# Kernel tuning notes

Hardware: AMD Instinct MI355X
Metric: run time of the kernel (lower is better)

The kernel has to match this reference:

```python
import jax, jax.numpy as jnp
import numpy as np

H = 2048

def setup_inputs() -> dict:
    key = jax.random.key(0)
    ks = jax.random.split(key, 7)
    s = 1.0 / np.sqrt(H)
    return {
        "input": jax.random.normal(ks[0], (2, 4096, H), dtype=jnp.float32),
        "Wq": jax.random.uniform(ks[1], (H, H), jnp.float32, -s, s),
        "bq": jax.random.uniform(ks[2], (H,), jnp.float32, -s, s),
        "Wk": jax.random.uniform(ks[3], (H, H), jnp.float32, -s, s),
        "bk": jax.random.uniform(ks[4], (H,), jnp.float32, -s, s),
        "Wv": jax.random.uniform(ks[5], (H, H), jnp.float32, -s, s),
        "bv": jax.random.uniform(ks[6], (H,), jnp.float32, -s, s),
    }

def reference(input, Wq, bq, Wk, bk, Wv, bv):
    # Linear projections: y = x @ W^T + b (torch nn.Linear convention)
    q = jnp.einsum('bsh,oh->bso', input, Wq) + bq
    k = jnp.einsum('bsh,oh->bso', input, Wk) + bk
    v = jnp.einsum('bsh,oh->bso', input, Wv) + bv
    # NOTE: original module has NO 1/sqrt(d) scaling and NO mask
    scores = jnp.einsum('bqh,bkh->bqk', q, k)          # [B,S,S]
    attn = jax.nn.softmax(scores, axis=-1)
    out = jnp.einsum('bqk,bkh->bqh', attn, v)           # [B,S,H]
    return out
```

## Files before the change

kernel.cpp:

```cpp
#include <hip/hip_runtime.h>
#include <hip/hip_bf16.h>
#include <cstdint>
#include <cstddef>


typedef _Float16 half8 __attribute__((ext_vector_type(8)));
typedef _Float16 half4 __attribute__((ext_vector_type(4)));
typedef float    f32x4 __attribute__((ext_vector_type(4)));

__device__ __forceinline__ void gld_lds16(const void* g, void* l) {
  __builtin_amdgcn_global_load_lds(
      (const __attribute__((address_space(1))) unsigned int*)g,
      (__attribute__((address_space(3))) unsigned int*)l, 16, 0, 0);
}

#define FENCE()  asm volatile("" ::: "memory")
#define LGKM(n)  asm volatile("s_waitcnt lgkmcnt(" #n ")" ::: "memory")
#define VMC(n)   asm volatile("s_waitcnt vmcnt(" #n ")" ::: "memory")
#define SBAR()   do { __builtin_amdgcn_s_barrier(); FENCE(); } while (0)
#define SCHED0() __builtin_amdgcn_sched_barrier(0)
#define PRIO1()  __builtin_amdgcn_s_setprio(1)
#define PRIO0()  __builtin_amdgcn_s_setprio(0)

#define LOAD_A(dst, RB, MH) do {                                            \
  const char* _p = ldsA + ((RB)*2 + wr) * 16384 + fr * 128;                 \
  _Pragma("unroll") for (int mi = 0; mi < 4; ++mi) {                        \
    dst[mi][0] = *(const half8*)(_p + ((MH)*4 + mi) * 2048 + cS0);          \
    dst[mi][1] = *(const half8*)(_p + ((MH)*4 + mi) * 2048 + cS1);          \
  }                                                                         \
} while (0)

#define LOAD_B(dst, RB, NH) do {                                            \
  const char* _p = ldsB + ((RB)*2 + (wc >> 1)) * 16384 +                    \
                   ((wc & 1) * 64 + fr) * 128;                              \
  _Pragma("unroll") for (int ni = 0; ni < 2; ++ni) {                        \
    dst[ni][0] = *(const half8*)(_p + ((NH)*2 + ni) * 2048 + cS0);          \
    dst[ni][1] = *(const half8*)(_p + ((NH)*2 + ni) * 2048 + cS1);          \
  }                                                                         \
} while (0)

#define MFMA_Q(AF, BF, MH, NH)                                              \
  _Pragma("unroll") for (int mi = 0; mi < 4; ++mi)                          \
  _Pragma("unroll") for (int ni = 0; ni < 2; ++ni) {                        \
    f32x4& _c = acc[(MH)*4 + mi][(NH)*2 + ni];                              \
    _c = __builtin_amdgcn_mfma_f32_16x16x32_f16(AF[mi][0], BF[ni][0], _c, 0, 0, 0); \
    _c = __builtin_amdgcn_mfma_f32_16x16x32_f16(AF[mi][1], BF[ni][1], _c, 0, 0, 0); \
  }

#define STAGE_A(bsel, h, kof)                                               \
  {                                                                         \
    const _Float16* _s = Abase + (size_t)((h) * 128) * lda + (kof);         \
    char* _d = ldsA + ((bsel)*2 + (h)) * 16384 + wvd;                       \
    gld_lds16(_s, _d);                                                      \
    gld_lds16(_s + lda8, _d + 1024);                                        \
  }
#define STAGE_B(bsel, h, kof)                                               \
  {                                                                         \
    const _Float16* _s = Bbase + (size_t)((h) * 128) * ldb + (kof);         \
    char* _d = ldsB + ((bsel)*2 + (h)) * 16384 + wvd;                       \
    gld_lds16(_s, _d);                                                      \
    gld_lds16(_s + ldb8, _d + 1024);                                        \
  }

template <int MODE>
__global__ __launch_bounds__(512) void gemm256(
    const _Float16* __restrict__ A, int lda,
    const _Float16* __restrict__ B, int ldb,
    const float* __restrict__ bias, const float* __restrict__ bias2,
    const float* __restrict__ bias3,
    void* __restrict__ out, void* __restrict__ out2, void* __restrict__ out3,
    int ldo, int K, size_t sA, size_t sB, size_t sO)
{
  __shared__ __attribute__((aligned(128))) char lds[131072];
  char* ldsA = (char*)lds;
  char* ldsB = (char*)lds + 65536;

  const int tid  = threadIdx.x;
  const int wv   = tid >> 6;
  const int lane = tid & 63;
  const int wr = wv >> 2;
  const int wc = wv & 3;
  const int bm = blockIdx.x * 256;
  const int bn = blockIdx.y * 256;
  A += (size_t)blockIdx.z * sA;
  B += (size_t)blockIdx.z * sB;

  const int fr = lane & 15;
  const int kq = lane >> 4;
  const int sx = (fr & 7) << 4;
  const int cS0 = (kq * 16) ^ sx;
  const int cS1 = (64 + kq * 16) ^ sx;
  const int lr  = lane >> 3;
  const int sc8 = ((lane & 7) ^ (lr & 7)) << 3;

  const _Float16* Abase = A + (size_t)(bm + wv * 16 + lr) * lda + sc8;
  const _Float16* Bbase = B + (size_t)(bn + wv * 16 + lr) * ldb + sc8;
  const size_t lda8 = (size_t)lda * 8, ldb8 = (size_t)ldb * 8;
  const int wvd = wv * 2048;

  f32x4 acc[8][4];
  const f32x4 zf = {0.f, 0.f, 0.f, 0.f};
#pragma unroll
  for (int mi = 0; mi < 8; ++mi)
#pragma unroll
    for (int ni = 0; ni < 4; ++ni) acc[mi][ni] = zf;

  half8 af[4][2], bf0[2][2], bf1[2][2];

  const int NT = K >> 6;
  const int NI = NT >> 1;

  STAGE_A(0, 0, 0); STAGE_A(0, 1, 0); STAGE_B(0, 0, 0); STAGE_B(0, 1, 0);
  STAGE_B(1, 0, 64); STAGE_B(1, 1, 64);
  VMC(4);
  SBAR();

  for (int it = 0; it < NI; ++it) {
    const bool more = (it < NI - 1);
    const size_t t1k = (size_t)(2 * it + 1) * 64;
    const size_t t2k = t1k + 64;
    const size_t t3k = t1k + 128;

    LOAD_A(af, 0, 0); LOAD_B(bf0, 0, 0);
    STAGE_A(1, 0, t1k);
    LGKM(8);
    SBAR(); LGKM(0); SCHED0();
    PRIO1(); MFMA_Q(af, bf0, 0, 0); PRIO0();
    SBAR();
    LOAD_B(bf1, 0, 1);
    STAGE_A(1, 1, t1k);
    SBAR(); LGKM(0); SCHED0();
    PRIO1(); MFMA_Q(af, bf1, 0, 1); PRIO0();
    SBAR();
    LOAD_A(af, 0, 1);
    if (more) STAGE_B(0, 0, t2k);
    SBAR(); LGKM(0); SCHED0();
    PRIO1(); MFMA_Q(af, bf1, 1, 1); PRIO0();
    SBAR();
    if (more) STAGE_B(0, 1, t2k);
    SBAR(); SCHED0();
    PRIO1(); MFMA_Q(af, bf0, 1, 0); PRIO0();
    if (more) { VMC(4); } else { VMC(0); }
    SBAR();

    LOAD_A(af, 1, 0); LOAD_B(bf0, 1, 0);
    if (more) STAGE_A(0, 0, t2k);
    LGKM(8);
    SBAR(); LGKM(0); SCHED0();
    PRIO1(); MFMA_Q(af, bf0, 0, 0); PRIO0();
    SBAR();
    LOAD_B(bf1, 1, 1);
    if (more) STAGE_A(0, 1, t2k);
    SBAR(); LGKM(0); SCHED0();
    PRIO1(); MFMA_Q(af, bf1, 0, 1); PRIO0();
    SBAR();
    LOAD_A(af, 1, 1);
    if (more) STAGE_B(1, 0, t3k);
    SBAR(); LGKM(0); SCHED0();
    PRIO1(); MFMA_Q(af, bf1, 1, 1); PRIO0();
    SBAR();
    if (more) STAGE_B(1, 1, t3k);
    SBAR(); SCHED0();
    PRIO1(); MFMA_Q(af, bf0, 1, 0); PRIO0();
    if (more) { VMC(4); } else { VMC(0); }
    SBAR();
  }

  if constexpr (MODE == 1) {
    const int seg = blockIdx.y >> 3;
    const int cb  = (blockIdx.y & 7) * 256;
    _Float16* O; const float* bp;
    if (seg == 0)      { O = (_Float16*)out;  bp = bias;  }
    else if (seg == 1) { O = (_Float16*)out2; bp = bias2; }
    else               { O = (_Float16*)out3; bp = bias3; }
#pragma unroll
    for (int mi = 0; mi < 8; ++mi) {
#pragma unroll
      for (int ni = 0; ni < 4; ++ni) {
        const int colL = cb + wc * 64 + ni * 16 + fr;
        const int row0 = bm + wr * 128 + mi * 16 + kq * 4;
        const f32x4 a = acc[mi][ni];
        const float bb = bp[colL];
        if (seg < 2) {
#pragma unroll
          for (int j = 0; j < 4; ++j)
            O[(size_t)(row0 + j) * 2048 + colL] = (_Float16)(a[j] + bb);
        } else {
          half4 h;
#pragma unroll
          for (int j = 0; j < 4; ++j) h[j] = (_Float16)(a[j] + bb);
          *(half4*)(O + (size_t)colL * 8192 + row0) = h;
        }
      }
    }
  } else {
#pragma unroll
    for (int mi = 0; mi < 8; ++mi) {
#pragma unroll
      for (int ni = 0; ni < 4; ++ni) {
        const int col  = bn + wc * 64 + ni * 16 + fr;
        const int row0 = bm + wr * 128 + mi * 16 + kq * 4;
        const f32x4 a = acc[mi][ni];
        if constexpr (MODE == 0) {
          float* O = (float*)out + (size_t)blockIdx.z * sO;
#pragma unroll
          for (int j = 0; j < 4; ++j) O[(size_t)(row0 + j) * ldo + col] = a[j];
        } else {
          _Float16* O = (_Float16*)out + (size_t)blockIdx.z * sO;
#pragma unroll
          for (int j = 0; j < 4; ++j)
            O[(size_t)(row0 + j) * ldo + col] = (_Float16)a[j];
        }
      }
    }
  }
}

__device__ __forceinline__ float wave_max_f(float v) {
#pragma unroll
  for (int o = 32; o; o >>= 1) v = fmaxf(v, __shfl_xor(v, o));
  return v;
}
__device__ __forceinline__ float wave_sum_f(float v) {
#pragma unroll
  for (int o = 32; o; o >>= 1) v += __shfl_xor(v, o);
  return v;
}

__global__ __launch_bounds__(256) void softmax_rows(
    const _Float16* __restrict__ S, _Float16* __restrict__ P)
{
  __shared__ float rmax[4], rsum[4];
  const int tid = threadIdx.x;
  const _Float16* s = S + (size_t)blockIdx.x * 4096;
  _Float16*       p = P + (size_t)blockIdx.x * 4096;

  const half8 v0 = ((const half8*)s)[tid];
  const half8 v1 = ((const half8*)s)[tid + 256];
  float f[16];
#pragma unroll
  for (int j = 0; j < 8; ++j) { f[j] = (float)v0[j]; f[8 + j] = (float)v1[j]; }

  float m = f[0];
#pragma unroll
  for (int j = 1; j < 16; ++j) m = fmaxf(m, f[j]);
  m = wave_max_f(m);
  if ((tid & 63) == 0) rmax[tid >> 6] = m;
  __syncthreads();
  m = fmaxf(fmaxf(rmax[0], rmax[1]), fmaxf(rmax[2], rmax[3]));

  float sum = 0.f;
#pragma unroll
  for (int j = 0; j < 16; ++j) { f[j] = __expf(f[j] - m); sum += f[j]; }
  sum = wave_sum_f(sum);
  if ((tid & 63) == 0) rsum[tid >> 6] = sum;
  __syncthreads();
  sum = rsum[0] + rsum[1] + rsum[2] + rsum[3];
  const float inv = 1.0f / sum;

  half8 o0, o1;
#pragma unroll
  for (int j = 0; j < 8; ++j) {
    o0[j] = (_Float16)(f[j] * inv);
    o1[j] = (_Float16)(f[8 + j] * inv);
  }
  ((half8*)p)[tid] = o0;
  ((half8*)p)[tid + 256] = o1;
}

__global__ __launch_bounds__(256) void cvt_all(
    const float* __restrict__ X,  const float* __restrict__ Wq,
    const float* __restrict__ Wk, const float* __restrict__ Wv,
    _Float16* __restrict__ dst, int nX4, int nW4)
{
  const int total = nX4 + 3 * nW4;
  const int stride = gridDim.x * 256;
  for (int idx = blockIdx.x * 256 + threadIdx.x; idx < total; idx += stride) {
    const float* src; int off;
    if (idx < nX4)                { src = X;  off = idx; }
    else if (idx < nX4 + nW4)     { src = Wq; off = idx - nX4; }
    else if (idx < nX4 + 2 * nW4) { src = Wk; off = idx - nX4 - nW4; }
    else                          { src = Wv; off = idx - nX4 - 2 * nW4; }
    const f32x4 x = ((const f32x4*)src)[off];
    half4 h;
#pragma unroll
    for (int j = 0; j < 4; ++j) h[j] = (_Float16)x[j];
    ((half4*)dst)[idx] = h;
  }
}

extern "C" void kernel_launch(void* const* d_in, const int* in_sizes, int n_in,
                              void* d_out, int out_size, void* d_ws, size_t ws_size,
                              hipStream_t stream)
{
  const float* X  = (const float*)d_in[0];
  const float* Wq = (const float*)d_in[1];
  const float* bq = (const float*)d_in[2];
  const float* Wk = (const float*)d_in[3];
  const float* bk = (const float*)d_in[4];
  const float* Wv = (const float*)d_in[5];
  const float* bv = (const float*)d_in[6];
  float* out = (float*)d_out;

  const size_t NX = (size_t)2 * 4096 * 2048;
  const size_t NW = (size_t)2048 * 2048;
  const size_t NS = (size_t)2 * 4096 * 4096;

  char* w = (char*)d_ws;
  _Float16* Ssc = (_Float16*)w;
  _Float16* Xh  = (_Float16*)w;
  _Float16* Wc  = (_Float16*)(w + NX * 2);
  _Float16* Q   = (_Float16*)(w + NS * 4);
  _Float16* Kp  = (_Float16*)(w + NS * 4 + NX * 2);
  _Float16* P   = (_Float16*)(w + NS * 4);
  _Float16* Vt  = (_Float16*)(w + NS * 4 + 2 * NX * 2);

  cvt_all<<<2048, 256, 0, stream>>>(X, Wq, Wk, Wv, Xh,
                                    (int)(NX / 4), (int)(NW / 4));

  const dim3 blk(512);
  gemm256<1><<<dim3(32, 24, 1), blk, 0, stream>>>(
      Xh, 2048, Wc, 2048, bq, bk, bv, Q, Kp, Vt, 2048, 2048, 0, 0, 0);
  gemm256<3><<<dim3(16, 16, 2), blk, 0, stream>>>(
      Q, 2048, Kp, 2048, nullptr, nullptr, nullptr, Ssc, nullptr, nullptr,
      4096, 2048, (size_t)4096 * 2048, (size_t)4096 * 2048,
      (size_t)4096 * 4096);
  softmax_rows<<<8192, 256, 0, stream>>>(Ssc, P);
  gemm256<0><<<dim3(16, 8, 2), blk, 0, stream>>>(
      P, 4096, Vt, 8192, nullptr, nullptr, nullptr, out, nullptr, nullptr,
      2048, 4096, (size_t)4096 * 4096, (size_t)4096, (size_t)4096 * 2048);
}
```

Baseline: 477.5 us.

## Switch GEMM inner product from 16x16x32 to 32x32x16 MFMA tiles

Replaces the 16x16x32 f16 MFMA fragments with 32x32x16 MFMA instructions, reorganising LDS fragment loads, accumulator layout (f32x16) and the epilogue index mapping to match. Larger MFMA tiles halve the number of LDS fragment reads per FLOP and reduce instruction issue overhead. The pipeline schedule and barriers are kept the same, with added sched barriers in the prologue. Risks include higher register pressure and different LDS bank-conflict behaviour with the new swizzle offsets.

```diff
diff --git a/kernel.cpp b/kernel.cpp
--- a/kernel.cpp
+++ b/kernel.cpp
@@ -6,7 +6,8 @@
 
 typedef _Float16 half8 __attribute__((ext_vector_type(8)));
 typedef _Float16 half4 __attribute__((ext_vector_type(4)));
-typedef float    f32x4 __attribute__((ext_vector_type(4)));
+typedef float    f32x4  __attribute__((ext_vector_type(4)));
+typedef float    f32x16 __attribute__((ext_vector_type(16)));
 
 __device__ __forceinline__ void gld_lds16(const void* g, void* l) {
   __builtin_amdgcn_global_load_lds(
@@ -22,30 +23,25 @@
 #define PRIO1()  __builtin_amdgcn_s_setprio(1)
 #define PRIO0()  __builtin_amdgcn_s_setprio(0)
 
-#define LOAD_A(dst, RB, MH) do {                                            \
-  const char* _p = ldsA + ((RB)*2 + wr) * 16384 + fr * 128;                 \
-  _Pragma("unroll") for (int mi = 0; mi < 4; ++mi) {                        \
-    dst[mi][0] = *(const half8*)(_p + ((MH)*4 + mi) * 2048 + cS0);          \
-    dst[mi][1] = *(const half8*)(_p + ((MH)*4 + mi) * 2048 + cS1);          \
-  }                                                                         \
+#define LOAD_A32(dst, RB, MP) do {                                          \
+  const char* _p = ldsA + ((RB)*2 + wr) * 16384 + ((MP)*64 + la31) * 128;   \
+  _Pragma("unroll") for (int mi = 0; mi < 2; ++mi)                          \
+    _Pragma("unroll") for (int s = 0; s < 4; ++s)                           \
+      dst[mi][s] = *(const half8*)(_p + mi * 4096 + cK[s]);                 \
 } while (0)
 
-#define LOAD_B(dst, RB, NH) do {                                            \
+#define LOAD_B32(dst, RB, NF) do {                                          \
   const char* _p = ldsB + ((RB)*2 + (wc >> 1)) * 16384 +                    \
-                   ((wc & 1) * 64 + fr) * 128;                              \
-  _Pragma("unroll") for (int ni = 0; ni < 2; ++ni) {                        \
-    dst[ni][0] = *(const half8*)(_p + ((NH)*2 + ni) * 2048 + cS0);          \
-    dst[ni][1] = *(const half8*)(_p + ((NH)*2 + ni) * 2048 + cS1);          \
-  }                                                                         \
+                   ((wc & 1) * 64 + (NF)*32 + la31) * 128;                  \
+  _Pragma("unroll") for (int s = 0; s < 4; ++s)                             \
+    dst[s] = *(const half8*)(_p + cK[s]);                                   \
 } while (0)
 
-#define MFMA_Q(AF, BF, MH, NH)                                              \
-  _Pragma("unroll") for (int mi = 0; mi < 4; ++mi)                          \
-  _Pragma("unroll") for (int ni = 0; ni < 2; ++ni) {                        \
-    f32x4& _c = acc[(MH)*4 + mi][(NH)*2 + ni];                              \
-    _c = __builtin_amdgcn_mfma_f32_16x16x32_f16(AF[mi][0], BF[ni][0], _c, 0, 0, 0); \
-    _c = __builtin_amdgcn_mfma_f32_16x16x32_f16(AF[mi][1], BF[ni][1], _c, 0, 0, 0); \
-  }
+#define MFMAC(MP, AF, BF, NF)                                               \
+  _Pragma("unroll") for (int s = 0; s < 4; ++s)                             \
+  _Pragma("unroll") for (int mi = 0; mi < 2; ++mi)                          \
+    acc32[(MP)*2 + mi][NF] = __builtin_amdgcn_mfma_f32_32x32x16_f16(        \
+        AF[mi][s], BF[s], acc32[(MP)*2 + mi][NF], 0, 0, 0);
 
 #define STAGE_A(bsel, h, kof)                                               \
   {                                                                         \
@@ -85,11 +81,12 @@
   A += (size_t)blockIdx.z * sA;
   B += (size_t)blockIdx.z * sB;
 
-  const int fr = lane & 15;
-  const int kq = lane >> 4;
-  const int sx = (fr & 7) << 4;
-  const int cS0 = (kq * 16) ^ sx;
-  const int cS1 = (64 + kq * 16) ^ sx;
+  const int la31 = lane & 31;
+  const int hi   = lane >> 5;
+  int cK[4];
+#pragma unroll
+  for (int s = 0; s < 4; ++s)
+    cK[s] = (hi * 16 + s * 32) ^ ((la31 & 7) << 4);
   const int lr  = lane >> 3;
   const int sc8 = ((lane & 7) ^ (lr & 7)) << 3;
 
@@ -98,20 +95,23 @@
   const size_t lda8 = (size_t)lda * 8, ldb8 = (size_t)ldb * 8;
   const int wvd = wv * 2048;
 
-  f32x4 acc[8][4];
-  const f32x4 zf = {0.f, 0.f, 0.f, 0.f};
-#pragma unroll
-  for (int mi = 0; mi < 8; ++mi)
-#pragma unroll
-    for (int ni = 0; ni < 4; ++ni) acc[mi][ni] = zf;
-
-  half8 af[4][2], bf0[2][2], bf1[2][2];
+  f32x16 acc32[4][2];
+#pragma unroll
+  for (int mf = 0; mf < 4; ++mf)
+#pragma unroll
+    for (int nf = 0; nf < 2; ++nf)
+#pragma unroll
+      for (int e = 0; e < 16; ++e) acc32[mf][nf][e] = 0.f;
+
+  half8 af[2][4], bf0[4], bf1[4];
 
   const int NT = K >> 6;
   const int NI = NT >> 1;
 
   STAGE_A(0, 0, 0); STAGE_A(0, 1, 0); STAGE_B(0, 0, 0); STAGE_B(0, 1, 0);
+  SCHED0();
   STAGE_B(1, 0, 64); STAGE_B(1, 1, 64);
+  SCHED0();
   VMC(4);
   SBAR();
 
@@ -121,47 +121,47 @@
     const size_t t2k = t1k + 64;
     const size_t t3k = t1k + 128;
 
-    LOAD_A(af, 0, 0); LOAD_B(bf0, 0, 0);
+    LOAD_A32(af, 0, 0); LOAD_B32(bf0, 0, 0);
     STAGE_A(1, 0, t1k);
     LGKM(8);
     SBAR(); LGKM(0); SCHED0();
-    PRIO1(); MFMA_Q(af, bf0, 0, 0); PRIO0();
-    SBAR();
-    LOAD_B(bf1, 0, 1);
+    PRIO1(); MFMAC(0, af, bf0, 0); PRIO0();
+    SBAR();
+    LOAD_B32(bf1, 0, 1);
     STAGE_A(1, 1, t1k);
     SBAR(); LGKM(0); SCHED0();
-    PRIO1(); MFMA_Q(af, bf1, 0, 1); PRIO0();
-    SBAR();
-    LOAD_A(af, 0, 1);
+    PRIO1(); MFMAC(0, af, bf1, 1); PRIO0();
+    SBAR();
+    LOAD_A32(af, 0, 1);
     if (more) STAGE_B(0, 0, t2k);
     SBAR(); LGKM(0); SCHED0();
-    PRIO1(); MFMA_Q(af, bf1, 1, 1); PRIO0();
+    PRIO1(); MFMAC(1, af, bf1, 1); PRIO0();
     SBAR();
     if (more) STAGE_B(0, 1, t2k);
     SBAR(); SCHED0();
-    PRIO1(); MFMA_Q(af, bf0, 1, 0); PRIO0();
+    PRIO1(); MFMAC(1, af, bf0, 0); PRIO0();
     if (more) { VMC(4); } else { VMC(0); }
     SBAR();
 
-    LOAD_A(af, 1, 0); LOAD_B(bf0, 1, 0);
+    LOAD_A32(af, 1, 0); LOAD_B32(bf0, 1, 0);
     if (more) STAGE_A(0, 0, t2k);
     LGKM(8);
     SBAR(); LGKM(0); SCHED0();
-    PRIO1(); MFMA_Q(af, bf0, 0, 0); PRIO0();
-    SBAR();
-    LOAD_B(bf1, 1, 1);
+    PRIO1(); MFMAC(0, af, bf0, 0); PRIO0();
+    SBAR();
+    LOAD_B32(bf1, 1, 1);
     if (more) STAGE_A(0, 1, t2k);
     SBAR(); LGKM(0); SCHED0();
-    PRIO1(); MFMA_Q(af, bf1, 0, 1); PRIO0();
-    SBAR();
-    LOAD_A(af, 1, 1);
+    PRIO1(); MFMAC(0, af, bf1, 1); PRIO0();
+    SBAR();
+    LOAD_A32(af, 1, 1);
     if (more) STAGE_B(1, 0, t3k);
     SBAR(); LGKM(0); SCHED0();
-    PRIO1(); MFMA_Q(af, bf1, 1, 1); PRIO0();
+    PRIO1(); MFMAC(1, af, bf1, 1); PRIO0();
     SBAR();
     if (more) STAGE_B(1, 1, t3k);
     SBAR(); SCHED0();
-    PRIO1(); MFMA_Q(af, bf0, 1, 0); PRIO0();
+    PRIO1(); MFMAC(1, af, bf0, 0); PRIO0();
     if (more) { VMC(4); } else { VMC(0); }
     SBAR();
   }
@@ -174,42 +174,53 @@
     else if (seg == 1) { O = (_Float16*)out2; bp = bias2; }
     else               { O = (_Float16*)out3; bp = bias3; }
 #pragma unroll
-    for (int mi = 0; mi < 8; ++mi) {
-#pragma unroll
-      for (int ni = 0; ni < 4; ++ni) {
-        const int colL = cb + wc * 64 + ni * 16 + fr;
-        const int row0 = bm + wr * 128 + mi * 16 + kq * 4;
-        const f32x4 a = acc[mi][ni];
+    for (int mf = 0; mf < 4; ++mf) {
+#pragma unroll
+      for (int nf = 0; nf < 2; ++nf) {
+        const int colL = cb + wc * 64 + nf * 32 + la31;
+        const int rb   = bm + wr * 128 + mf * 32 + hi * 4;
+        const f32x16 a = acc32[mf][nf];
         const float bb = bp[colL];
         if (seg < 2) {
 #pragma unroll
-          for (int j = 0; j < 4; ++j)
-            O[(size_t)(row0 + j) * 2048 + colL] = (_Float16)(a[j] + bb);
+          for (int g = 0; g < 4; ++g)
+#pragma unroll
+            for (int j = 0; j < 4; ++j)
+              O[(size_t)(rb + 8 * g + j) * 2048 + colL] =
+                  (_Float16)(a[g * 4 + j] + bb);
         } else {
-          half4 h;
-#pragma unroll
-          for (int j = 0; j < 4; ++j) h[j] = (_Float16)(a[j] + bb);
-          *(half4*)(O + (size_t)colL * 8192 + row0) = h;
+#pragma unroll
+          for (int g = 0; g < 4; ++g) {
+            half4 h;
+#pragma unroll
+            for (int j = 0; j < 4; ++j) h[j] = (_Float16)(a[g * 4 + j] + bb);
+            *(half4*)(O + (size_t)colL * 8192 + rb + 8 * g) = h;
+          }
         }
       }
     }
   } else {
 #pragma unroll
-    for (int mi = 0; mi < 8; ++mi) {
-#pragma unroll
-      for (int ni = 0; ni < 4; ++ni) {
-        const int col  = bn + wc * 64 + ni * 16 + fr;
-        const int row0 = bm + wr * 128 + mi * 16 + kq * 4;
-        const f32x4 a = acc[mi][ni];
+    for (int mf = 0; mf < 4; ++mf) {
+#pragma unroll
+      for (int nf = 0; nf < 2; ++nf) {
+        const int col = bn + wc * 64 + nf * 32 + la31;
+        const int rb  = bm + wr * 128 + mf * 32 + hi * 4;
+        const f32x16 a = acc32[mf][nf];
         if constexpr (MODE == 0) {
           float* O = (float*)out + (size_t)blockIdx.z * sO;
 #pragma unroll
-          for (int j = 0; j < 4; ++j) O[(size_t)(row0 + j) * ldo + col] = a[j];
+          for (int g = 0; g < 4; ++g)
+#pragma unroll
+            for (int j = 0; j < 4; ++j)
+              O[(size_t)(rb + 8 * g + j) * ldo + col] = a[g * 4 + j];
         } else {
           _Float16* O = (_Float16*)out + (size_t)blockIdx.z * sO;
 #pragma unroll
-          for (int j = 0; j < 4; ++j)
-            O[(size_t)(row0 + j) * ldo + col] = (_Float16)a[j];
+          for (int g = 0; g < 4; ++g)
+#pragma unroll
+            for (int j = 0; j < 4; ++j)
+              O[(size_t)(rb + 8 * g + j) * ldo + col] = (_Float16)a[g * 4 + j];
         }
       }
     }
```

Result: slower. 540.4 us (+13.2%).
